# Performance work log

Hardware: AMD Instinct MI355X
Metric: run time of the kernel (lower is better)

## Reference

```python
import jax, jax.numpy as jnp
import numpy as np

DEPTH = 2
DIM = 256
MLP = 1024
B = 2
N = 2048


def setup_inputs() -> dict:
    key = jax.random.key(0)
    ks = jax.random.split(key, 6)
    s = 0.02
    d = DIM
    f32 = jnp.float32
    return {
        "x": jax.random.normal(ks[0], (B, N, d), f32),
        "ln1_g": jnp.ones((DEPTH, d), f32),
        "ln1_b": jnp.zeros((DEPTH, d), f32),
        "Wqkv": (jax.random.normal(ks[1], (DEPTH, d, 3 * d), f32) * s),
        "bqkv": jnp.zeros((DEPTH, 3 * d), f32),
        "Wo": (jax.random.normal(ks[2], (DEPTH, d, d), f32) * s),
        "bo": jnp.zeros((DEPTH, d), f32),
        "ln2_g": jnp.ones((DEPTH, d), f32),
        "ln2_b": jnp.zeros((DEPTH, d), f32),
        "W1": (jax.random.normal(ks[3], (DEPTH, d, MLP), f32) * s),
        "b1": jnp.zeros((DEPTH, MLP), f32),
        "W2": (jax.random.normal(ks[4], (DEPTH, MLP, d), f32) * s),
        "b2": jnp.zeros((DEPTH, d), f32),
        "heads": 8,
    }


def _ln(x, g, b, eps=1e-5):
    m = x.mean(-1, keepdims=True)
    v = ((x - m) ** 2).mean(-1, keepdims=True)
    return (x - m) * jax.lax.rsqrt(v + eps) * g + b


def reference(x, ln1_g, ln1_b, Wqkv, bqkv, Wo, bo, ln2_g, ln2_b, W1, b1, W2, b2, heads):
    b, n, dim = x.shape
    hd = dim // heads
    scale = hd ** -0.5
    depth = Wqkv.shape[0]
    out = x
    # NOTE: faithful to original: `x` is never updated inside the loop,
    # so only the last layer's output is returned.
    for i in range(depth):
        y = _ln(x, ln1_g[i], ln1_b[i])
        qkv = y @ Wqkv[i] + bqkv[i]                      # [b,n,3*dim]
        qkv = qkv.reshape(b, n, 3, heads, hd)
        q, k, v = jnp.moveaxis(qkv, 2, 0)                # each [b,n,h,hd]
        q = q.transpose(0, 2, 1, 3)                      # [b,h,n,hd]
        k = k.transpose(0, 2, 1, 3)
        v = v.transpose(0, 2, 1, 3)
        dots = jnp.einsum('bhid,bhjd->bhij', q, k) * scale
        attn = jax.nn.softmax(dots, axis=-1)
        o = jnp.einsum('bhij,bhjd->bhid', attn, v)       # [b,h,n,hd]
        o = o.transpose(0, 2, 1, 3).reshape(b, n, dim)
        o = o @ Wo[i] + bo[i]
        a = o + x                                        # attn residual
        z = _ln(a, ln2_g[i], ln2_b[i])
        m = jax.nn.gelu(z @ W1[i] + b1[i], approximate=False) @ W2[i] + b2[i]
        out = m + a                                      # mlp residual
    return out
```

## Files before the change

### kernel.cpp

```cpp
#include <hip/hip_runtime.h>
#include <hip/hip_bf16.h>
#include <math.h>

#define DEPTHC 2
#define DIMD   256
#define MLPD   1024
#define BB     2
#define NN     2048
#define HH     8
#define HD     32
#define ROWS   (BB * NN)

typedef __attribute__((ext_vector_type(8))) short bf16x8;
typedef __attribute__((ext_vector_type(4))) float f32x4;

__device__ __forceinline__ short f2bf(float x) {
    union { float f; unsigned u; } c; c.f = x;
    unsigned u = c.u + (0x7fffu + ((c.u >> 16) & 1u));
    return (short)(u >> 16);
}
__device__ __forceinline__ float bf2f(short s) {
    union { unsigned u; float f; } c; c.u = ((unsigned)(unsigned short)s) << 16;
    return c.f;
}

__global__ __launch_bounds__(256) void prep(
    const float* __restrict__ Wqkv, const float* __restrict__ Wo,
    const float* __restrict__ W1,   const float* __restrict__ W2,
    short* __restrict__ WqkvF, short* __restrict__ WoF,
    short* __restrict__ W1F,   short* __restrict__ W2F,
    const float* __restrict__ x, const float* __restrict__ g,
    const float* __restrict__ be, short* __restrict__ y)
{
    __shared__ short Ts[128][72];

    if (blockIdx.x >= 96) {
        const int wave = threadIdx.x >> 6;
        const int lane = threadIdx.x & 63;
        const int row  = (blockIdx.x - 96) * 4 + wave;
        const int c    = lane * 4;

        const float4 v = *(const float4*)&x[(size_t)row * DIMD + c];
        float s  = v.x + v.y + v.z + v.w;
        float sq = v.x * v.x + v.y * v.y + v.z * v.z + v.w * v.w;
#pragma unroll
        for (int off = 32; off > 0; off >>= 1) {
            s  += __shfl_down(s,  off, 64);
            sq += __shfl_down(sq, off, 64);
        }
        s  = __shfl(s,  0, 64);
        sq = __shfl(sq, 0, 64);

        const float mean = s * (1.f / DIMD);
        const float var  = sq * (1.f / DIMD) - mean * mean;
        const float rstd = rsqrtf(var + 1e-5f);

        const float4 gg = *(const float4*)&g[c];
        const float4 bb = *(const float4*)&be[c];
        short4 ov;
        ov.x = f2bf((v.x - mean) * rstd * gg.x + bb.x);
        ov.y = f2bf((v.y - mean) * rstd * gg.y + bb.y);
        ov.z = f2bf((v.z - mean) * rstd * gg.z + bb.z);
        ov.w = f2bf((v.w - mean) * rstd * gg.w + bb.w);
        *(short4*)&y[(size_t)row * DIMD + c] = ov;
        return;
    }

    int blk = blockIdx.x;
    const float* W; short* WF; int K, N;
    if (blk < 24)      {           W = Wqkv; WF = WqkvF; K = 256;  N = 768;  }
    else if (blk < 32) { blk -= 24; W = Wo;   WF = WoF;   K = 256;  N = 256;  }
    else if (blk < 64) { blk -= 32; W = W1;   WF = W1F;   K = 256;  N = 1024; }
    else               { blk -= 64; W = W2;   WF = W2F;   K = 1024; N = 256;  }
    const int nkc = K >> 7;
    const int bx  = blk / nkc;
    const int kc  = blk % nkc;
    const int n0  = bx * 64;
    const int k0  = kc * 128;

    const int nc  = threadIdx.x & 63;
    const int kr0 = threadIdx.x >> 6;
#pragma unroll
    for (int i = 0; i < 32; ++i) {
        const int kr = kr0 + i * 4;
        Ts[kr][nc] = f2bf(W[(size_t)(k0 + kr) * N + n0 + nc]);
    }
    __syncthreads();

    short* out = WF + ((size_t)bx * nkc + kc) * 8192;
#pragma unroll
    for (int i = 0; i < 4; ++i) {
        const int u    = threadIdx.x + i * 256;
        const int l16  = u & 15;
        const int quad = (u >> 4) & 3;
        const int nt   = (u >> 6) & 3;
        const int ks   = (u >> 8) & 3;
        const int n    = nt * 16 + l16;
        const int kk   = (ks * 4 + quad) * 8;
        bf16x8 v;
#pragma unroll
        for (int j = 0; j < 8; ++j) v[j] = Ts[kk + j][n];
        *(bf16x8*)&out[(size_t)u * 8] = v;
    }
}

template <int K, bool GELU, bool RES, bool OBF, bool VTG>
__global__ __launch_bounds__(256) void gemm_ks(
    const short* __restrict__ A, const short* __restrict__ WF,
    const float* __restrict__ bias, const float* __restrict__ R,
    void* __restrict__ Cv, int N, short* __restrict__ vtg)
{
    __shared__ short smem[4][4096];
    __shared__ short vts[64][66];

    const int tid  = threadIdx.x;
    const int w    = tid >> 6;
    const int lane = tid & 63;
    const int quad = lane >> 4;
    const int l16  = lane & 15;
    const int n0   = blockIdx.x * 64;
    const int m0   = blockIdx.y * 64;
    constexpr int NKC   = K / 128;
    constexpr int SLICE = K / 4;
    constexpr int NHC   = SLICE / 64;

    const short* wfb  = WF + (size_t)blockIdx.x * NKC * 8192;
    const short* arow = A + (size_t)(m0 + l16) * K + quad * 8;
    short* reg = smem[w];

    f32x4 acc[4][4] = {};

#pragma unroll
    for (int hc = 0; hc < NHC; ++hc) {
        const int kbase = w * SLICE + hc * 64;
        const short* src = wfb +
            ((size_t)(kbase >> 7) * 1024 + (size_t)((kbase >> 6) & 1) * 512) * 8;
#pragma unroll
        for (int i = 0; i < 8; ++i)
            *(bf16x8*)&reg[(i * 64 + lane) * 8] =
                *(const bf16x8*)&src[(size_t)(i * 64 + lane) * 8];

#pragma unroll
        for (int ksl = 0; ksl < 2; ++ksl) {
            const int kk = kbase + ksl * 32;
            bf16x8 af[4];
#pragma unroll
            for (int mt = 0; mt < 4; ++mt)
                af[mt] = *(const bf16x8*)(arow + (size_t)mt * 16 * K + kk);
#pragma unroll
            for (int nt = 0; nt < 4; ++nt) {
                const bf16x8 bf = *(const bf16x8*)
                    &reg[(((ksl * 4 + nt) * 4 + quad) * 16 + l16) * 8];
#pragma unroll
                for (int mt = 0; mt < 4; ++mt)
                    acc[mt][nt] = __builtin_amdgcn_mfma_f32_16x16x32_bf16(
                        af[mt], bf, acc[mt][nt], 0, 0, 0);
            }
        }
    }

#pragma unroll
    for (int p = 0; p < 2; ++p) {
        __syncthreads();
#pragma unroll
        for (int mtl = 0; mtl < 2; ++mtl)
#pragma unroll
            for (int nt = 0; nt < 4; ++nt)
                *(f32x4*)&smem[w][((mtl * 4 + nt) * 64 + lane) * 8] = acc[2 * p + mtl][nt];
        __syncthreads();
        if ((w >> 1) == p) {
            const int mtl = w & 1;
            const int mt  = 2 * p + mtl;
#pragma unroll
            for (int nt = 0; nt < 4; ++nt) {
                const int idx = ((mtl * 4 + nt) * 64 + lane) * 8;
                const f32x4 s0 = *(const f32x4*)&smem[0][idx];
                const f32x4 s1 = *(const f32x4*)&smem[1][idx];
                const f32x4 s2 = *(const f32x4*)&smem[2][idx];
                const f32x4 s3 = *(const f32x4*)&smem[3][idx];
                const f32x4 s  = (s0 + s1) + (s2 + s3);
                const int col  = n0 + nt * 16 + l16;
                const float bb = bias[col];
#pragma unroll
                for (int r = 0; r < 4; ++r) {
                    const int row = m0 + mt * 16 + quad * 4 + r;
                    float v = s[r] + bb;
                    if (RES)  v += R[(size_t)row * N + col];
                    if (GELU) v = 0.5f * v * (1.f + erff(v * 0.70710678118f));
                    const short bv = f2bf(v);
                    if (OBF) ((short*)Cv)[(size_t)row * N + col] = bv;
                    else     ((float*)Cv)[(size_t)row * N + col] = v;
                    if (VTG && n0 >= 2 * DIMD)
                        vts[row - m0][col - n0] = bv;
                }
            }
        }
    }

    if (VTG && n0 >= 2 * DIMD) {
        __syncthreads();
        const int vcol = tid >> 2;
        const int tseg = (tid & 3) * 16;
        const int vc   = n0 - 2 * DIMD + vcol;
        const int b    = m0 >> 11;
        const int q0v  = m0 & (NN - 1);
        const int h    = vc >> 5;
        const int d    = vc & 31;
        short tmp[16];
#pragma unroll
        for (int i = 0; i < 16; ++i) tmp[i] = vts[tseg + i][vcol];
        short* dst = &vtg[((size_t)(b * HH + h) * HD + d) * NN + q0v + tseg];
        *(bf16x8*)dst       = *(const bf16x8*)&tmp[0];
        *(bf16x8*)(dst + 8) = *(const bf16x8*)&tmp[8];
    }
}

__global__ __launch_bounds__(256) void attn_mfma(
    const short* __restrict__ qkv, const short* __restrict__ vtg,
    short* __restrict__ o)
{
    __shared__ __align__(16) short Ks2[2][64][40];
    __shared__ __align__(16) short Vs2[2][32][72];
    __shared__ __align__(16) short Ps[4][16][72];

    const int tid  = threadIdx.x;
    const int w    = tid >> 6;
    const int lane = tid & 63;
    const int quad = lane >> 4;
    const int l16  = lane & 15;
    const int qw    = w & 1;
    const int kside = w >> 1;
    const int bh   = blockIdx.y;
    const int b    = bh >> 3;
    const int h    = bh & 7;
    const int q0   = blockIdx.x * 32 + qw * 16;

    const float scale = 0.17677669529663689f;
    const float shift = 11.090354888959125f;
    const short* base = qkv + (size_t)b * NN * (3 * DIMD);

    const bf16x8 qfrag =
        *(const bf16x8*)(base + (size_t)(q0 + l16) * (3 * DIMD) + h * HD + quad * 8);

    const int side = tid >> 7;
    const int st   = tid & 127;
    const int kr   = st >> 1;
    const int kd   = (st & 1) * 16;
    const int vd   = st >> 2;
    const int vk0  = (st & 3) * 16;

    const short* kgp = base + (size_t)(side * 1024 + kr) * (3 * DIMD)
                       + DIMD + h * HD + kd;
    const short* vgp = vtg + ((size_t)bh * HD + vd) * NN + side * 1024 + vk0;

    f32x4 oacc0 = {0.f, 0.f, 0.f, 0.f};
    f32x4 oacc1 = {0.f, 0.f, 0.f, 0.f};
    float rowsum = 0.f;

    bf16x8 kr0 = *(const bf16x8*)kgp;
    bf16x8 kr1 = *(const bf16x8*)(kgp + 8);
    bf16x8 vr0 = *(const bf16x8*)vgp;
    bf16x8 vr1 = *(const bf16x8*)(vgp + 8);

#pragma unroll 1
    for (int t = 0; t < NN / 128; ++t) {
        __syncthreads();
        *(bf16x8*)&Ks2[side][kr][kd]     = kr0;
        *(bf16x8*)&Ks2[side][kr][kd + 8] = kr1;
        *(bf16x8*)&Vs2[side][vd][vk0]     = vr0;
        *(bf16x8*)&Vs2[side][vd][vk0 + 8] = vr1;
        __syncthreads();

        if (t + 1 < NN / 128) {
            const short* kn = kgp + (size_t)(t + 1) * 64 * (3 * DIMD);
            const short* vn = vgp + (t + 1) * 64;
            kr0 = *(const bf16x8*)kn;
            kr1 = *(const bf16x8*)(kn + 8);
            vr0 = *(const bf16x8*)vn;
            vr1 = *(const bf16x8*)(vn + 8);
        }

        f32x4 s[4];
#pragma unroll
        for (int kt = 0; kt < 4; ++kt) {
            const bf16x8 kf = *(const bf16x8*)&Ks2[kside][kt * 16 + l16][quad * 8];
            f32x4 z = {0.f, 0.f, 0.f, 0.f};
            s[kt] = __builtin_amdgcn_mfma_f32_16x16x32_bf16(kf, qfrag, z, 0, 0, 0);
        }

#pragma unroll
        for (int kt = 0; kt < 4; ++kt) {
            short4 pv;
#pragma unroll
            for (int r = 0; r < 4; ++r) {
                const float p = __expf(fmaf(s[kt][r], scale, -shift));
                rowsum += p;
                union { float f; unsigned u; } cv; cv.f = p;
                ((short*)&pv)[r] = (short)(cv.u >> 16);
            }
            *(short4*)&Ps[w][l16][kt * 16 + quad * 4] = pv;
        }

#pragma unroll
        for (int c = 0; c < 2; ++c) {
            const bf16x8 pf = *(const bf16x8*)&Ps[w][l16][c * 32 + quad * 8];
            const bf16x8 v0 = *(const bf16x8*)&Vs2[kside][l16][c * 32 + quad * 8];
            const bf16x8 v1 = *(const bf16x8*)&Vs2[kside][16 + l16][c * 32 + quad * 8];
            oacc0 = __builtin_amdgcn_mfma_f32_16x16x32_bf16(pf, v0, oacc0, 0, 0, 0);
            oacc1 = __builtin_amdgcn_mfma_f32_16x16x32_bf16(pf, v1, oacc1, 0, 0, 0);
        }
    }

    rowsum += __shfl_xor(rowsum, 16, 64);
    rowsum += __shfl_xor(rowsum, 32, 64);

    float* sc = (float*)&Ks2[0][0][0];
    __syncthreads();
    if (kside == 1) {
        float* o8 = sc + (size_t)(qw * 64 + lane) * 8;
        *(f32x4*)o8       = oacc0;
        *(f32x4*)(o8 + 4) = oacc1;
        if (lane < 16) sc[1024 + qw * 16 + lane] = rowsum;
    }
    __syncthreads();
    if (kside == 0) {
        const float* o8 = sc + (size_t)(qw * 64 + lane) * 8;
        oacc0 += *(const f32x4*)o8;
        oacc1 += *(const f32x4*)(o8 + 4);
        rowsum += sc[1024 + qw * 16 + l16];

#pragma unroll
        for (int r = 0; r < 4; ++r) {
            const float L   = __shfl(rowsum, quad * 4 + r, 16);
            const float inv = 1.f / L;
            const size_t row = (size_t)(b * NN + q0 + quad * 4 + r);
            o[row * DIMD + h * HD + l16]      = f2bf(oacc0[r] * inv);
            o[row * DIMD + h * HD + 16 + l16] = f2bf(oacc1[r] * inv);
        }
    }
}

__global__ __launch_bounds__(1024) void tail_fused(
    const short* __restrict__ obf, const float* __restrict__ x,
    const short* __restrict__ WoF, const float* __restrict__ bo,
    const float* __restrict__ ln2g, const float* __restrict__ ln2b,
    const short* __restrict__ W1F, const float* __restrict__ b1,
    const short* __restrict__ W2F, const float* __restrict__ b2,
    float* __restrict__ out)
{
    __shared__ __align__(16) float aS[16][264];
    __shared__ __align__(16) short zS[16][264];
    __shared__ __align__(16) short mS[16][1032];

    const int tid  = threadIdx.x;
    const int w    = tid >> 6;
    const int lane = tid & 63;
    const int quad = lane >> 4;
    const int l16  = lane & 15;
    const int m0   = blockIdx.x * 16;

    {
        const short* arow   = obf + (size_t)(m0 + l16) * DIMD + quad * 8;
        const short* wchunk = WoF + (size_t)(w >> 2) * 2 * 8192;
        const int ntl = w & 3;
        f32x4 acc = {};
#pragma unroll
        for (int ks = 0; ks < 8; ++ks) {
            const int k = ks * 32;
            const bf16x8 af = *(const bf16x8*)(arow + k);
            const int ub = (k >> 7) * 1024 + ((k >> 5) & 3) * 256 + quad * 16 + l16;
            const bf16x8 bf = *(const bf16x8*)&wchunk[(size_t)(ub + ntl * 64) * 8];
            acc = __builtin_amdgcn_mfma_f32_16x16x32_bf16(af, bf, acc, 0, 0, 0);
        }
        const int col  = w * 16 + l16;
        const float bb = bo[col];
#pragma unroll
        for (int r = 0; r < 4; ++r) {
            const int row = quad * 4 + r;
            aS[row][col] = acc[r] + bb + x[(size_t)(m0 + row) * DIMD + col];
        }
    }
    __syncthreads();

    {
        const int row = w;
        const int c4  = lane * 4;
        const float4 v = *(const float4*)&aS[row][c4];
        float s  = v.x + v.y + v.z + v.w;
        float sq = v.x * v.x + v.y * v.y + v.z * v.z + v.w * v.w;
#pragma unroll
        for (int off = 32; off > 0; off >>= 1) {
            s  += __shfl_xor(s,  off, 64);
            sq += __shfl_xor(sq, off, 64);
        }
        const float mean = s * (1.f / DIMD);
        const float var  = sq * (1.f / DIMD) - mean * mean;
        const float rstd = rsqrtf(var + 1e-5f);
        const float4 gg = *(const float4*)&ln2g[c4];
        const float4 bb = *(const float4*)&ln2b[c4];
        short4 ov;
        ov.x = f2bf((v.x - mean) * rstd * gg.x + bb.x);
        ov.y = f2bf((v.y - mean) * rstd * gg.y + bb.y);
        ov.z = f2bf((v.z - mean) * rstd * gg.z + bb.z);
        ov.w = f2bf((v.w - mean) * rstd * gg.w + bb.w);
        *(short4*)&zS[row][c4] = ov;
    }
    __syncthreads();

    {
        f32x4 acc[4] = {};
#pragma unroll
        for (int ks = 0; ks < 8; ++ks) {
            const int k = ks * 32;
            const bf16x8 af = *(const bf16x8*)&zS[l16][k + quad * 8];
            const int ub = (k >> 7) * 1024 + ((k >> 5) & 3) * 256 + quad * 16 + l16;
#pragma unroll
            for (int nt = 0; nt < 4; ++nt) {
                const bf16x8 bf = *(const bf16x8*)
                    &W1F[(size_t)w * 2 * 8192 + (size_t)(ub + nt * 64) * 8];
                acc[nt] = __builtin_amdgcn_mfma_f32_16x16x32_bf16(af, bf, acc[nt], 0, 0, 0);
            }
        }
#pragma unroll
        for (int nt = 0; nt < 4; ++nt) {
            const int col  = w * 64 + nt * 16 + l16;
            const float bb = b1[col];
#pragma unroll
            for (int r = 0; r < 4; ++r) {
                float v = acc[nt][r] + bb;
                v = 0.5f * v * (1.f + erff(v * 0.70710678118f));
                mS[quad * 4 + r][col] = f2bf(v);
            }
        }
    }
    __syncthreads();

    {
        f32x4 acc = {};
        const short* wchunk = W2F + (size_t)(w >> 2) * 8 * 8192;
        const int ntl = w & 3;
#pragma unroll
        for (int ks = 0; ks < 32; ++ks) {
            const int k = ks * 32;
            const bf16x8 af = *(const bf16x8*)&mS[l16][k + quad * 8];
            const int ub = (k >> 7) * 1024 + ((k >> 5) & 3) * 256 + quad * 16 + l16;
            const bf16x8 bf = *(const bf16x8*)&wchunk[(size_t)(ub + ntl * 64) * 8];
            acc = __builtin_amdgcn_mfma_f32_16x16x32_bf16(af, bf, acc, 0, 0, 0);
        }
        const int col  = w * 16 + l16;
        const float bb = b2[col];
#pragma unroll
        for (int r = 0; r < 4; ++r) {
            const int row = quad * 4 + r;
            out[(size_t)(m0 + row) * DIMD + col] = acc[r] + bb + aS[row][col];
        }
    }
}

extern "C" void kernel_launch(void* const* d_in, const int* in_sizes, int n_in,
                              void* d_out, int out_size, void* d_ws, size_t ws_size,
                              hipStream_t stream)
{
    const int L = DEPTHC - 1;
    const float* x     = (const float*)d_in[0];
    const float* ln1_g = (const float*)d_in[1]  + L * DIMD;
    const float* ln1_b = (const float*)d_in[2]  + L * DIMD;
    const float* Wqkv  = (const float*)d_in[3]  + (size_t)L * DIMD * 3 * DIMD;
    const float* bqkv  = (const float*)d_in[4]  + L * 3 * DIMD;
    const float* Wo    = (const float*)d_in[5]  + (size_t)L * DIMD * DIMD;
    const float* bo    = (const float*)d_in[6]  + L * DIMD;
    const float* ln2_g = (const float*)d_in[7]  + L * DIMD;
    const float* ln2_b = (const float*)d_in[8]  + L * DIMD;
    const float* W1    = (const float*)d_in[9]  + (size_t)L * DIMD * MLPD;
    const float* b1    = (const float*)d_in[10] + L * MLPD;
    const float* W2    = (const float*)d_in[11] + (size_t)L * MLPD * DIMD;
    const float* b2    = (const float*)d_in[12] + L * DIMD;
    float* out = (float*)d_out;

    short* WqkvF = (short*)d_ws;
    short* WoF   = WqkvF + 12 * 2 * 8192;
    short* W1F   = WoF   + 4 * 2 * 8192;
    short* W2F   = W1F   + 16 * 2 * 8192;
    short* ybf   = W2F   + 4 * 8 * 8192;
    short* qkvbf = ybf   + (size_t)ROWS * DIMD;
    short* vtg   = qkvbf + (size_t)ROWS * 3 * DIMD;
    short* obf   = vtg   + (size_t)16 * HD * NN;

    prep<<<96 + ROWS / 4, 256, 0, stream>>>(
        Wqkv, Wo, W1, W2, WqkvF, WoF, W1F, W2F, x, ln1_g, ln1_b, ybf);

    gemm_ks<256, false, false, true, true><<<dim3(12, 64), 256, 0, stream>>>(
        ybf, WqkvF, bqkv, nullptr, qkvbf, 3 * DIMD, vtg);

    attn_mfma<<<dim3(NN / 32, BB * HH), 256, 0, stream>>>(qkvbf, vtg, obf);

    tail_fused<<<ROWS / 16, 1024, 0, stream>>>(
        obf, x, WoF, bo, ln2_g, ln2_b, W1F, b1, W2F, b2, out);
}
```

Measured before the change: 141.5 us.

## Write Q and K in head-major packed layout from QKV GEMM epilogue

The QKV GEMM epilogue now stages every output tile in shared memory and writes Q and K as contiguous per-head [bh][token][32] buffers, in addition to the existing transposed V, instead of a strided row-major qkv matrix. The attention kernel then reads Q fragments and K tiles from these packed buffers, so each K row load is contiguous rather than strided by 768 elements. The K shared-memory row pitch also changes from 40 to 44, which may affect bank conflicts. In exchange, the GEMM does an extra shared-memory staging pass and a barrier for the Q and K tiles.

```diff
diff --git a/kernel.cpp b/kernel.cpp
--- a/kernel.cpp
+++ b/kernel.cpp
@@ -18,10 +18,6 @@
     union { float f; unsigned u; } c; c.f = x;
     unsigned u = c.u + (0x7fffu + ((c.u >> 16) & 1u));
     return (short)(u >> 16);
-}
-__device__ __forceinline__ float bf2f(short s) {
-    union { unsigned u; float f; } c; c.u = ((unsigned)(unsigned short)s) << 16;
-    return c.f;
 }
 
 __global__ __launch_bounds__(256) void prep(
@@ -108,7 +104,8 @@
 __global__ __launch_bounds__(256) void gemm_ks(
     const short* __restrict__ A, const short* __restrict__ WF,
     const float* __restrict__ bias, const float* __restrict__ R,
-    void* __restrict__ Cv, int N, short* __restrict__ vtg)
+    void* __restrict__ Cv, int N,
+    short* __restrict__ qpk, short* __restrict__ kpk, short* __restrict__ vtg)
 {
     __shared__ short smem[4][4096];
     __shared__ short vts[64][66];
@@ -188,38 +185,57 @@
                     if (RES)  v += R[(size_t)row * N + col];
                     if (GELU) v = 0.5f * v * (1.f + erff(v * 0.70710678118f));
                     const short bv = f2bf(v);
-                    if (OBF) ((short*)Cv)[(size_t)row * N + col] = bv;
-                    else     ((float*)Cv)[(size_t)row * N + col] = v;
-                    if (VTG && n0 >= 2 * DIMD)
+                    if (VTG) {
                         vts[row - m0][col - n0] = bv;
+                    } else if (OBF) {
+                        ((short*)Cv)[(size_t)row * N + col] = bv;
+                    } else {
+                        ((float*)Cv)[(size_t)row * N + col] = v;
+                    }
                 }
             }
         }
     }
 
-    if (VTG && n0 >= 2 * DIMD) {
+    if (VTG) {
         __syncthreads();
-        const int vcol = tid >> 2;
-        const int tseg = (tid & 3) * 16;
-        const int vc   = n0 - 2 * DIMD + vcol;
-        const int b    = m0 >> 11;
-        const int q0v  = m0 & (NN - 1);
-        const int h    = vc >> 5;
-        const int d    = vc & 31;
-        short tmp[16];
-#pragma unroll
-        for (int i = 0; i < 16; ++i) tmp[i] = vts[tseg + i][vcol];
-        short* dst = &vtg[((size_t)(b * HH + h) * HD + d) * NN + q0v + tseg];
-        *(bf16x8*)dst       = *(const bf16x8*)&tmp[0];
-        *(bf16x8*)(dst + 8) = *(const bf16x8*)&tmp[8];
+        const int b   = m0 >> 11;
+        const int q0v = m0 & (NN - 1);
+        if (n0 < 2 * DIMD) {
+            short* dstb = (n0 < DIMD) ? qpk : kpk;
+            const int bc   = n0 & (DIMD - 1);
+            const int tok  = tid >> 2;
+            const int dseg = (tid & 3) * 16;
+            const int c = bc + dseg;
+            const int h = c >> 5;
+            const int d = c & 31;
+            short tmp[16];
+#pragma unroll
+            for (int i = 0; i < 16; ++i) tmp[i] = vts[tok][dseg + i];
+            short* dst = dstb + ((size_t)(b * HH + h) * NN + q0v + tok) * HD + d;
+            *(bf16x8*)dst       = *(const bf16x8*)&tmp[0];
+            *(bf16x8*)(dst + 8) = *(const bf16x8*)&tmp[8];
+        } else {
+            const int vcol = tid >> 2;
+            const int tseg = (tid & 3) * 16;
+            const int vc   = n0 - 2 * DIMD + vcol;
+            const int h    = vc >> 5;
+            const int d    = vc & 31;
+            short tmp[16];
+#pragma unroll
+            for (int i = 0; i < 16; ++i) tmp[i] = vts[tseg + i][vcol];
+            short* dst = &vtg[((size_t)(b * HH + h) * HD + d) * NN + q0v + tseg];
+            *(bf16x8*)dst       = *(const bf16x8*)&tmp[0];
+            *(bf16x8*)(dst + 8) = *(const bf16x8*)&tmp[8];
+        }
     }
 }
 
 __global__ __launch_bounds__(256) void attn_mfma(
-    const short* __restrict__ qkv, const short* __restrict__ vtg,
-    short* __restrict__ o)
+    const short* __restrict__ qpk, const short* __restrict__ kpk,
+    const short* __restrict__ vtg, short* __restrict__ o)
 {
-    __shared__ __align__(16) short Ks2[2][64][40];
+    __shared__ __align__(16) short Ks2[2][64][44];
     __shared__ __align__(16) short Vs2[2][32][72];
     __shared__ __align__(16) short Ps[4][16][72];
 
@@ -237,10 +253,9 @@
 
     const float scale = 0.17677669529663689f;
     const float shift = 11.090354888959125f;
-    const short* base = qkv + (size_t)b * NN * (3 * DIMD);
 
     const bf16x8 qfrag =
-        *(const bf16x8*)(base + (size_t)(q0 + l16) * (3 * DIMD) + h * HD + quad * 8);
+        *(const bf16x8*)(qpk + ((size_t)bh * NN + q0 + l16) * HD + quad * 8);
 
     const int side = tid >> 7;
     const int st   = tid & 127;
@@ -249,8 +264,7 @@
     const int vd   = st >> 2;
     const int vk0  = (st & 3) * 16;
 
-    const short* kgp = base + (size_t)(side * 1024 + kr) * (3 * DIMD)
-                       + DIMD + h * HD + kd;
+    const short* kgp = kpk + ((size_t)bh * NN + side * 1024 + kr) * HD + kd;
     const short* vgp = vtg + ((size_t)bh * HD + vd) * NN + side * 1024 + vk0;
 
     f32x4 oacc0 = {0.f, 0.f, 0.f, 0.f};
@@ -272,7 +286,7 @@
         __syncthreads();
 
         if (t + 1 < NN / 128) {
-            const short* kn = kgp + (size_t)(t + 1) * 64 * (3 * DIMD);
+            const short* kn = kgp + (size_t)(t + 1) * 64 * HD;
             const short* vn = vgp + (t + 1) * 64;
             kr0 = *(const bf16x8*)kn;
             kr1 = *(const bf16x8*)(kn + 8);
@@ -482,17 +496,18 @@
     short* W1F   = WoF   + 4 * 2 * 8192;
     short* W2F   = W1F   + 16 * 2 * 8192;
     short* ybf   = W2F   + 4 * 8 * 8192;
-    short* qkvbf = ybf   + (size_t)ROWS * DIMD;
-    short* vtg   = qkvbf + (size_t)ROWS * 3 * DIMD;
+    short* qpk   = ybf   + (size_t)ROWS * DIMD;
+    short* kpk   = qpk   + (size_t)16 * NN * HD;
+    short* vtg   = kpk   + (size_t)16 * NN * HD;
     short* obf   = vtg   + (size_t)16 * HD * NN;
 
     prep<<<96 + ROWS / 4, 256, 0, stream>>>(
         Wqkv, Wo, W1, W2, WqkvF, WoF, W1F, W2F, x, ln1_g, ln1_b, ybf);
 
-    gemm_ks<256, false, false, true, true><<<dim3(12, 64), 256, 0, stream>>>(
-        ybf, WqkvF, bqkv, nullptr, qkvbf, 3 * DIMD, vtg);
-
-    attn_mfma<<<dim3(NN / 32, BB * HH), 256, 0, stream>>>(qkvbf, vtg, obf);
+    gemm_ks<256, false, false, false, true><<<dim3(12, 64), 256, 0, stream>>>(
+        ybf, WqkvF, bqkv, nullptr, nullptr, 3 * DIMD, qpk, kpk, vtg);
+
+    attn_mfma<<<dim3(NN / 32, BB * HH), 256, 0, stream>>>(qpk, kpk, vtg, obf);
 
     tail_fused<<<ROWS / 16, 1024, 0, stream>>>(
         obf, x, WoF, bo, ln2_g, ln2_b, W1F, b1, W2F, b2, out);
```

Measured after the change: 139.6 us. About the same (-1.3%).
